# Optimization experiments

Measured on AMD Instinct MI355X. Metric: run time of the kernel, lower is better.

## Reference

```python
import jax, jax.numpy as jnp
import numpy as np

B, S, NUM_TYPES, NUM_NODES, FREQ = 8, 2048, 8, 32, 256
COMP_R, COMP_L, COMP_C = 0, 1, 2
LS = 0.1  # label smoothing
W_TYPE, W_NODE, W_VAL, W_IMP, W_D1, W_D2, W_SELF, W_DUP = 1.0, 1.0, 0.5, 1.0, 0.5, 0.3, 2.0, 1.0


def setup_inputs() -> dict:
    key = jax.random.key(0)
    ks = jax.random.split(key, 9)
    type_logits = jax.random.normal(ks[0], (B, S, NUM_TYPES), jnp.float32)
    node_a_logits = jax.random.normal(ks[1], (B, S, NUM_NODES), jnp.float32)
    node_b_logits = jax.random.normal(ks[2], (B, S, NUM_NODES), jnp.float32)
    values = jax.random.normal(ks[3], (B, S, 1), jnp.float32)
    t_type = jax.random.randint(ks[4], (B, S, 1), 0, NUM_TYPES)
    t_na = jax.random.randint(ks[5], (B, S, 1), 0, NUM_NODES)
    t_nb = jax.random.randint(ks[6], (B, S, 1), 0, NUM_NODES)
    t_val = jax.random.normal(ks[7], (B, S, 1), jnp.float32)
    target_seq = jnp.concatenate(
        [t_type.astype(jnp.float32), t_na.astype(jnp.float32), t_nb.astype(jnp.float32), t_val], axis=-1)
    ki = jax.random.split(ks[8], 2)
    pred_impedance = jax.random.normal(ki[0], (B, 2, FREQ), jnp.float32)
    target_impedance = jax.random.normal(ki[1], (B, 2, FREQ), jnp.float32)
    return {"type_logits": type_logits, "node_a_logits": node_a_logits,
            "node_b_logits": node_b_logits, "values": values, "target_seq": target_seq,
            "pred_impedance": pred_impedance, "target_impedance": target_impedance}


def _ce_smooth(logits, targets):
    # torch CrossEntropyLoss(label_smoothing=LS), mean reduction
    logp = jax.nn.log_softmax(logits, axis=-1)
    nll = -jnp.take_along_axis(logp, targets[..., None], axis=-1)[..., 0]
    smooth = -jnp.mean(logp, axis=-1)
    return jnp.mean((1.0 - LS) * nll + LS * smooth)


def _mse(a, b):
    return jnp.mean((a - b) ** 2)


def _losses(type_logits, node_a_logits, node_b_logits, values,
            pred_impedance, target_impedance, target_seq):
    target_types = target_seq[:, :, 0].astype(jnp.int32)
    target_na = target_seq[:, :, 1].astype(jnp.int32)
    target_nb = target_seq[:, :, 2].astype(jnp.int32)
    target_values = target_seq[:, :, 3:4]

    type_loss = _ce_smooth(type_logits, target_types)
    node_a_loss = _ce_smooth(node_a_logits, target_na)
    node_b_loss = _ce_smooth(node_b_logits, target_nb)
    value_loss = _mse(values, target_values)

    # validity penalties
    pa = jax.nn.softmax(node_a_logits, axis=-1)  # [B,S,N]
    pb = jax.nn.softmax(node_b_logits, axis=-1)
    pt = jax.nn.softmax(type_logits, axis=-1)
    comp_mask = pt[:, :, COMP_R] + pt[:, :, COMP_L] + pt[:, :, COMP_C]  # [B,S]

    selfloop_prob = jnp.sum(pa * pb, axis=-1)  # [B,S]
    selfloop_penalty = jnp.mean(selfloop_prob * comp_mask)

    # edge_probs[b,s] = outer(pa,pb) + outer(pa,pb).T, flattened to [B,S,N*N]
    outer = jnp.einsum('bsi,bsj->bsij', pa, pb)
    edge = (outer + jnp.swapaxes(outer, -1, -2)).reshape(B, S, NUM_NODES * NUM_NODES)
    em = edge * comp_mask[..., None]  # fold comp weight into edge vectors
    gram = jnp.einsum('bsk,btk->bst', em, em)  # [B,S,S]
    trace = jnp.einsum('bss->b', gram)
    pair_sum = 0.5 * (jnp.sum(gram) - jnp.sum(trace))
    duplicate_penalty = pair_sum / (B * S * (S - 1) / 2 + 1e-8)

    # impedance derivative losses
    pm, tm = pred_impedance[:, 0, :], target_impedance[:, 0, :]
    pp, tp = pred_impedance[:, 1, :], target_impedance[:, 1, :]
    mag_loss = _mse(pm, tm)
    pd1, td1 = pm[:, 1:] - pm[:, :-1], tm[:, 1:] - tm[:, :-1]
    d1_loss = _mse(pd1, td1)
    d2_loss = _mse(pd1[:, 1:] - pd1[:, :-1], td1[:, 1:] - td1[:, :-1])
    phase_loss = _mse(pp, tp)

    total = (W_TYPE * type_loss + W_NODE * (node_a_loss + node_b_loss)
             + W_VAL * value_loss + W_SELF * selfloop_penalty
             + W_DUP * duplicate_penalty + W_IMP * mag_loss
             + W_D1 * d1_loss + W_D2 * d2_loss + 0.1 * phase_loss)
    return (total, type_loss, node_a_loss, node_b_loss, value_loss,
            selfloop_penalty, duplicate_penalty, mag_loss, d1_loss, d2_loss, phase_loss)


def reference(type_logits, node_a_logits, node_b_logits, values, target_seq,
              pred_impedance, target_impedance):
    return _losses(type_logits, node_a_logits, node_b_logits, values,
                   pred_impedance, target_impedance, target_seq)
```

## Files before the change

kernel.cpp:

```cpp
#include <hip/hip_runtime.h>


#define BB 8
#define SS 2048
#define NT 8
#define NN 32
#define FQ 256
#define NPOS (BB*SS)
#define NBLK 256
#define WS_USLOT 0
#define WS_SSLOT (NBLK*1024)
#define WS_BATCH (WS_SSLOT + NBLK*8)

constexpr float LS_ = 0.1f;

__device__ __forceinline__ float softmax32(const float* __restrict__ src, int pos,
                                           int tgt, float* __restrict__ p) {
    const float4* q = reinterpret_cast<const float4*>(src) + pos * 8;
    #pragma unroll
    for (int i = 0; i < 8; i++) {
        float4 v = q[i];
        p[4*i] = v.x; p[4*i+1] = v.y; p[4*i+2] = v.z; p[4*i+3] = v.w;
    }
    float mx = p[0], sx = 0.f, pt = 0.f;
    #pragma unroll
    for (int i = 0; i < NN; i++) { mx = fmaxf(mx, p[i]); sx += p[i]; }
    #pragma unroll
    for (int i = 0; i < NN; i++) { pt = (i == tgt) ? p[i] : pt; }
    float es = 0.f;
    #pragma unroll
    for (int i = 0; i < NN; i++) { float e = expf(p[i] - mx); p[i] = e; es += e; }
    const float inv = 1.f / es;
    #pragma unroll
    for (int i = 0; i < NN; i++) p[i] *= inv;
    const float logZ = mx + logf(es);
    return (1.f - LS_) * (logZ - pt) + LS_ * (logZ - sx * (1.f / NN));
}

__global__ __launch_bounds__(64) void ck_main(
    const float* __restrict__ type_logits,
    const float* __restrict__ na_logits,
    const float* __restrict__ nb_logits,
    const float* __restrict__ values,
    const float* __restrict__ target_seq,
    float* __restrict__ ws)
{
    const int tid = threadIdx.x;
    const int bid = blockIdx.x;
    const int b   = bid >> 5;
    const int s   = ((bid & 31) << 6) + tid;
    const int pos = b * SS + s;

    const float4 tg = reinterpret_cast<const float4*>(target_seq)[pos];
    const int tt = (int)tg.x;
    const int ta = (int)tg.y;
    const int tb = (int)tg.z;
    const float tv = tg.w;

    float x[NT];
    {
        const float4* p = reinterpret_cast<const float4*>(type_logits) + pos * 2;
        float4 v0 = p[0], v1 = p[1];
        x[0]=v0.x; x[1]=v0.y; x[2]=v0.z; x[3]=v0.w;
        x[4]=v1.x; x[5]=v1.y; x[6]=v1.z; x[7]=v1.w;
    }
    float xmax = x[0], xs = 0.f, xt = 0.f;
    #pragma unroll
    for (int i = 0; i < NT; i++) { xmax = fmaxf(xmax, x[i]); xs += x[i]; }
    #pragma unroll
    for (int i = 0; i < NT; i++) { xt = (i == tt) ? x[i] : xt; }
    float es = 0.f, e012 = 0.f;
    #pragma unroll
    for (int i = 0; i < NT; i++) {
        float e = expf(x[i] - xmax);
        es += e;
        if (i < 3) e012 += e;
    }
    const float logZt = xmax + logf(es);
    const float lt = (1.f - LS_) * (logZt - xt) + LS_ * (logZt - xs * (1.f / NT));
    const float m = e012 / es;

    float pa[NN], pb[NN];
    const float la = softmax32(na_logits, pos, ta, pa);
    const float lb = softmax32(nb_logits, pos, tb, pb);

    float Sa = 0.f, Sb = 0.f, dot = 0.f;
    #pragma unroll
    for (int i = 0; i < NN; i++) {
        Sa = fmaf(pa[i], pa[i], Sa);
        Sb = fmaf(pb[i], pb[i], Sb);
        dot = fmaf(pa[i], pb[i], dot);
    }
    const float self = m * dot;
    const float tr   = 2.f * m * m * (Sa * Sb + dot * dot);
    const float dv   = values[pos] - tv;
    const float vsq  = dv * dv;

    float r0 = lt, r1 = la, r2 = lb, r3 = vsq, r4 = self, r5 = tr;
    #pragma unroll
    for (int o = 32; o > 0; o >>= 1) {
        r0 += __shfl_down(r0, o); r1 += __shfl_down(r1, o);
        r2 += __shfl_down(r2, o); r3 += __shfl_down(r3, o);
        r4 += __shfl_down(r4, o); r5 += __shfl_down(r5, o);
    }
    if (tid == 0) {
        float* sp = ws + WS_SSLOT + bid * 8;
        sp[0]=r0; sp[1]=r1; sp[2]=r2; sp[3]=r3; sp[4]=r4; sp[5]=r5;
    }

    __shared__ float4 lpa[64][9];
    __shared__ float4 lpb[64][9];
    #pragma unroll
    for (int q = 0; q < 8; q++) {
        lpa[tid][q] = make_float4(m*pa[4*q], m*pa[4*q+1], m*pa[4*q+2], m*pa[4*q+3]);
        lpb[tid][q] = make_float4(pb[4*q], pb[4*q+1], pb[4*q+2], pb[4*q+3]);
    }
    __syncthreads();

    const int i4 = tid >> 3;
    const int j4 = tid & 7;
    float acc[4][4];
    #pragma unroll
    for (int ii = 0; ii < 4; ii++)
        #pragma unroll
        for (int jj = 0; jj < 4; jj++) acc[ii][jj] = 0.f;
    for (int t = 0; t < 64; t++) {
        float4 av = lpa[t][i4];
        float4 bv = lpb[t][j4];
        const float aa[4] = {av.x, av.y, av.z, av.w};
        const float bbv[4] = {bv.x, bv.y, bv.z, bv.w};
        #pragma unroll
        for (int ii = 0; ii < 4; ii++)
            #pragma unroll
            for (int jj = 0; jj < 4; jj++)
                acc[ii][jj] = fmaf(aa[ii], bbv[jj], acc[ii][jj]);
    }
    float4* slot = reinterpret_cast<float4*>(ws + WS_USLOT + bid * 1024);
    #pragma unroll
    for (int ii = 0; ii < 4; ii++)
        slot[((i4*4+ii)*32 + j4*4) >> 2] =
            make_float4(acc[ii][0], acc[ii][1], acc[ii][2], acc[ii][3]);
}

__device__ __forceinline__ float blk_reduce256(float v, float* lds) {
    #pragma unroll
    for (int o = 32; o > 0; o >>= 1) v += __shfl_down(v, o);
    const int tid = threadIdx.x;
    __syncthreads();
    if ((tid & 63) == 0) lds[tid >> 6] = v;
    __syncthreads();
    return lds[0] + lds[1] + lds[2] + lds[3];
}

__global__ __launch_bounds__(256) void ck_batch(
    const float* __restrict__ pred_imp,
    const float* __restrict__ targ_imp,
    float* __restrict__ ws)
{
    const int tid = threadIdx.x;
    const int b   = blockIdx.x;
    __shared__ float Ub[1024];
    __shared__ float red[4];

    float ua = 0.f, ub = 0.f, uc = 0.f, ud = 0.f;
    const float* base = ws + WS_USLOT + (size_t)b * 32 * 1024;
    for (int sl = 0; sl < 32; sl++) {
        const float* p = base + sl * 1024;
        ua += p[tid];
        ub += p[tid + 256];
        uc += p[tid + 512];
        ud += p[tid + 768];
    }
    Ub[tid]       = ua;
    Ub[tid + 256] = ub;
    Ub[tid + 512] = uc;
    Ub[tid + 768] = ud;
    __syncthreads();

    float gr = 0.f;
    #pragma unroll
    for (int r = 0; r < 4; r++) {
        const int e = tid + r * 256;
        const int i = e >> 5, j = e & 31;
        const float u  = Ub[e];
        const float ut = Ub[(j << 5) | i];
        gr = fmaf(u, u, gr);
        gr = fmaf(u, ut, gr);
    }

    const float* pm = pred_imp + b * 2 * FQ;
    const float* tm = targ_imp + b * 2 * FQ;
    const int f = tid;
    const float p0 = pm[f], t0 = tm[f];
    const float dm = p0 - t0;
    const float dp = pm[FQ + f] - tm[FQ + f];
    float mag = dm * dm;
    float phs = dp * dp;
    float d1 = 0.f, d2 = 0.f;
    if (f < FQ - 1) {
        const float p1 = pm[f + 1], t1 = tm[f + 1];
        const float a = (p1 - p0) - (t1 - t0);
        d1 = a * a;
        if (f < FQ - 2) {
            const float p2 = pm[f + 2], t2 = tm[f + 2];
            const float c = (p2 - 2.f*p1 + p0) - (t2 - 2.f*t1 + t0);
            d2 = c * c;
        }
    }

    float s0=0.f, s1=0.f, s2=0.f, s3=0.f, s4=0.f, s5=0.f;
    if (tid < 32) {
        const float* sp = ws + WS_SSLOT + (b * 32 + tid) * 8;
        s0 = sp[0]; s1 = sp[1]; s2 = sp[2]; s3 = sp[3]; s4 = sp[4]; s5 = sp[5];
    }

    const float GR  = blk_reduce256(gr,  red);
    const float MAG = blk_reduce256(mag, red);
    const float PHS = blk_reduce256(phs, red);
    const float D1  = blk_reduce256(d1,  red);
    const float D2  = blk_reduce256(d2,  red);
    const float S0  = blk_reduce256(s0,  red);
    const float S1  = blk_reduce256(s1,  red);
    const float S2  = blk_reduce256(s2,  red);
    const float S3  = blk_reduce256(s3,  red);
    const float S4  = blk_reduce256(s4,  red);
    const float S5  = blk_reduce256(s5,  red);

    if (tid == 0) {
        float* o = ws + WS_BATCH + b * 16;
        o[0]=GR; o[1]=MAG; o[2]=PHS; o[3]=D1; o[4]=D2;
        o[5]=S0; o[6]=S1; o[7]=S2; o[8]=S3; o[9]=S4; o[10]=S5;
    }
}

__global__ __launch_bounds__(64) void ck_out(const float* __restrict__ ws,
                                             float* __restrict__ out)
{
    if (threadIdx.x != 0) return;
    float GR=0,MAG=0,PHS=0,D1=0,D2=0,S0=0,S1=0,S2=0,S3=0,S4=0,S5=0;
    #pragma unroll
    for (int b = 0; b < BB; b++) {
        const float* p = ws + WS_BATCH + b * 16;
        GR+=p[0]; MAG+=p[1]; PHS+=p[2]; D1+=p[3]; D2+=p[4];
        S0+=p[5]; S1+=p[6]; S2+=p[7]; S3+=p[8]; S4+=p[9]; S5+=p[10];
    }
    const float invN = 1.f / (float)NPOS;
    const float type_loss = S0 * invN;
    const float na_loss   = S1 * invN;
    const float nb_loss   = S2 * invN;
    const float val_loss  = S3 * invN;
    const float self_p    = S4 * invN;
    const float trace     = S5;
    const float sum_gram  = 2.f * GR;
    const float pair_sum  = 0.5f * (sum_gram - trace);
    const float dup   = pair_sum / ((float)BB * SS * (SS - 1) * 0.5f + 1e-8f);
    const float mag_l = MAG / (float)(BB * FQ);
    const float d1_l  = D1  / (float)(BB * (FQ - 1));
    const float d2_l  = D2  / (float)(BB * (FQ - 2));
    const float ph_l  = PHS / (float)(BB * FQ);
    const float total = 1.0f * type_loss + 1.0f * (na_loss + nb_loss)
                      + 0.5f * val_loss + 2.0f * self_p + 1.0f * dup
                      + 1.0f * mag_l + 0.5f * d1_l + 0.3f * d2_l + 0.1f * ph_l;
    out[0]=total; out[1]=type_loss; out[2]=na_loss; out[3]=nb_loss;
    out[4]=val_loss; out[5]=self_p; out[6]=dup; out[7]=mag_l;
    out[8]=d1_l; out[9]=d2_l; out[10]=ph_l;
}

extern "C" void kernel_launch(void* const* d_in, const int* in_sizes, int n_in,
                              void* d_out, int out_size, void* d_ws, size_t ws_size,
                              hipStream_t stream)
{
    const float* type_logits = (const float*)d_in[0];
    const float* na_logits   = (const float*)d_in[1];
    const float* nb_logits   = (const float*)d_in[2];
    const float* values      = (const float*)d_in[3];
    const float* target_seq  = (const float*)d_in[4];
    const float* pred_imp    = (const float*)d_in[5];
    const float* targ_imp    = (const float*)d_in[6];
    float* out = (float*)d_out;
    float* ws  = (float*)d_ws;

    ck_main<<<NBLK, 64, 0, stream>>>(type_logits, na_logits, nb_logits,
                                     values, target_seq, ws);
    ck_batch<<<BB, 256, 0, stream>>>(pred_imp, targ_imp, ws);
    ck_out<<<1, 64, 0, stream>>>(ws, out);
}
```

Measured before the change: 81.35 us.

## Fold final reduction into batch kernel via atomic ticket; pack two waves per block

Removes the third single-thread output kernel by having the last finishing batch block (detected with an atomic ticket counter plus thread fences) compute the final losses. ck_main now runs two independent wavefronts per 128-thread block, halving the block count while keeping per-wave slot layout. The intent is to cut one kernel launch and its inter-kernel gap. It adds a reset of the ticket inside ck_main and relies on correct fence ordering across blocks.

New measurement: 83.65 us. 1.03x slower.

```diff
diff --git a/kernel.cpp b/kernel.cpp
--- a/kernel.cpp
+++ b/kernel.cpp
@@ -7,10 +7,11 @@
 #define NN 32
 #define FQ 256
 #define NPOS (BB*SS)
-#define NBLK 256
+#define NSLOT 256
 #define WS_USLOT 0
-#define WS_SSLOT (NBLK*1024)
-#define WS_BATCH (WS_SSLOT + NBLK*8)
+#define WS_SSLOT (NSLOT*1024)
+#define WS_BATCH (WS_SSLOT + NSLOT*8)
+#define WS_TICKET (WS_BATCH + BB*16)
 
 constexpr float LS_ = 0.1f;
 
@@ -37,7 +38,7 @@
     return (1.f - LS_) * (logZ - pt) + LS_ * (logZ - sx * (1.f / NN));
 }
 
-__global__ __launch_bounds__(64) void ck_main(
+__global__ __launch_bounds__(128) void ck_main(
     const float* __restrict__ type_logits,
     const float* __restrict__ na_logits,
     const float* __restrict__ nb_logits,
@@ -45,11 +46,18 @@
     const float* __restrict__ target_seq,
     float* __restrict__ ws)
 {
-    const int tid = threadIdx.x;
-    const int bid = blockIdx.x;
-    const int b   = bid >> 5;
-    const int s   = ((bid & 31) << 6) + tid;
-    const int pos = b * SS + s;
+    const int tid  = threadIdx.x;
+    const int bid  = blockIdx.x;
+    const int w    = tid >> 6;
+    const int lane = tid & 63;
+    const int gw   = bid * 2 + w;
+    const int b    = gw >> 5;
+    const int s    = ((gw & 31) << 6) + lane;
+    const int pos  = b * SS + s;
+
+    if (tid == 0 && bid == 0) {
+        *reinterpret_cast<int*>(ws + WS_TICKET) = 0;
+    }
 
     const float4 tg = reinterpret_cast<const float4*>(target_seq)[pos];
     const int tt = (int)tg.x;
@@ -103,30 +111,30 @@
         r2 += __shfl_down(r2, o); r3 += __shfl_down(r3, o);
         r4 += __shfl_down(r4, o); r5 += __shfl_down(r5, o);
     }
-    if (tid == 0) {
-        float* sp = ws + WS_SSLOT + bid * 8;
+    if (lane == 0) {
+        float* sp = ws + WS_SSLOT + gw * 8;
         sp[0]=r0; sp[1]=r1; sp[2]=r2; sp[3]=r3; sp[4]=r4; sp[5]=r5;
     }
 
-    __shared__ float4 lpa[64][9];
-    __shared__ float4 lpb[64][9];
+    __shared__ float4 lpa[2][64][9];
+    __shared__ float4 lpb[2][64][9];
     #pragma unroll
     for (int q = 0; q < 8; q++) {
-        lpa[tid][q] = make_float4(m*pa[4*q], m*pa[4*q+1], m*pa[4*q+2], m*pa[4*q+3]);
-        lpb[tid][q] = make_float4(pb[4*q], pb[4*q+1], pb[4*q+2], pb[4*q+3]);
-    }
-    __syncthreads();
-
-    const int i4 = tid >> 3;
-    const int j4 = tid & 7;
+        lpa[w][lane][q] = make_float4(m*pa[4*q], m*pa[4*q+1], m*pa[4*q+2], m*pa[4*q+3]);
+        lpb[w][lane][q] = make_float4(pb[4*q], pb[4*q+1], pb[4*q+2], pb[4*q+3]);
+    }
+    __syncthreads();
+
+    const int i4 = lane >> 3;
+    const int j4 = lane & 7;
     float acc[4][4];
     #pragma unroll
     for (int ii = 0; ii < 4; ii++)
         #pragma unroll
         for (int jj = 0; jj < 4; jj++) acc[ii][jj] = 0.f;
     for (int t = 0; t < 64; t++) {
-        float4 av = lpa[t][i4];
-        float4 bv = lpb[t][j4];
+        float4 av = lpa[w][t][i4];
+        float4 bv = lpb[w][t][j4];
         const float aa[4] = {av.x, av.y, av.z, av.w};
         const float bbv[4] = {bv.x, bv.y, bv.z, bv.w};
         #pragma unroll
@@ -135,7 +143,7 @@
             for (int jj = 0; jj < 4; jj++)
                 acc[ii][jj] = fmaf(aa[ii], bbv[jj], acc[ii][jj]);
     }
-    float4* slot = reinterpret_cast<float4*>(ws + WS_USLOT + bid * 1024);
+    float4* slot = reinterpret_cast<float4*>(ws + WS_USLOT + gw * 1024);
     #pragma unroll
     for (int ii = 0; ii < 4; ii++)
         slot[((i4*4+ii)*32 + j4*4) >> 2] =
@@ -155,7 +163,8 @@
 __global__ __launch_bounds__(256) void ck_batch(
     const float* __restrict__ pred_imp,
     const float* __restrict__ targ_imp,
-    float* __restrict__ ws)
+    float* __restrict__ ws,
+    float* __restrict__ out)
 {
     const int tid = threadIdx.x;
     const int b   = blockIdx.x;
@@ -230,40 +239,41 @@
         float* o = ws + WS_BATCH + b * 16;
         o[0]=GR; o[1]=MAG; o[2]=PHS; o[3]=D1; o[4]=D2;
         o[5]=S0; o[6]=S1; o[7]=S2; o[8]=S3; o[9]=S4; o[10]=S5;
-    }
-}
-
-__global__ __launch_bounds__(64) void ck_out(const float* __restrict__ ws,
-                                             float* __restrict__ out)
-{
-    if (threadIdx.x != 0) return;
-    float GR=0,MAG=0,PHS=0,D1=0,D2=0,S0=0,S1=0,S2=0,S3=0,S4=0,S5=0;
-    #pragma unroll
-    for (int b = 0; b < BB; b++) {
-        const float* p = ws + WS_BATCH + b * 16;
-        GR+=p[0]; MAG+=p[1]; PHS+=p[2]; D1+=p[3]; D2+=p[4];
-        S0+=p[5]; S1+=p[6]; S2+=p[7]; S3+=p[8]; S4+=p[9]; S5+=p[10];
-    }
-    const float invN = 1.f / (float)NPOS;
-    const float type_loss = S0 * invN;
-    const float na_loss   = S1 * invN;
-    const float nb_loss   = S2 * invN;
-    const float val_loss  = S3 * invN;
-    const float self_p    = S4 * invN;
-    const float trace     = S5;
-    const float sum_gram  = 2.f * GR;
-    const float pair_sum  = 0.5f * (sum_gram - trace);
-    const float dup   = pair_sum / ((float)BB * SS * (SS - 1) * 0.5f + 1e-8f);
-    const float mag_l = MAG / (float)(BB * FQ);
-    const float d1_l  = D1  / (float)(BB * (FQ - 1));
-    const float d2_l  = D2  / (float)(BB * (FQ - 2));
-    const float ph_l  = PHS / (float)(BB * FQ);
-    const float total = 1.0f * type_loss + 1.0f * (na_loss + nb_loss)
-                      + 0.5f * val_loss + 2.0f * self_p + 1.0f * dup
-                      + 1.0f * mag_l + 0.5f * d1_l + 0.3f * d2_l + 0.1f * ph_l;
-    out[0]=total; out[1]=type_loss; out[2]=na_loss; out[3]=nb_loss;
-    out[4]=val_loss; out[5]=self_p; out[6]=dup; out[7]=mag_l;
-    out[8]=d1_l; out[9]=d2_l; out[10]=ph_l;
+
+        __threadfence();
+        int* ticket = reinterpret_cast<int*>(ws + WS_TICKET);
+        const int old = atomicAdd(ticket, 1);
+        if (old == BB - 1) {
+            __threadfence();
+            float GRt=0,MAGt=0,PHSt=0,D1t=0,D2t=0,T0=0,T1=0,T2=0,T3=0,T4=0,T5=0;
+            #pragma unroll
+            for (int k = 0; k < BB; k++) {
+                const float* p = ws + WS_BATCH + k * 16;
+                GRt+=p[0]; MAGt+=p[1]; PHSt+=p[2]; D1t+=p[3]; D2t+=p[4];
+                T0+=p[5]; T1+=p[6]; T2+=p[7]; T3+=p[8]; T4+=p[9]; T5+=p[10];
+            }
+            const float invN = 1.f / (float)NPOS;
+            const float type_loss = T0 * invN;
+            const float na_loss   = T1 * invN;
+            const float nb_loss   = T2 * invN;
+            const float val_loss  = T3 * invN;
+            const float self_p    = T4 * invN;
+            const float trace     = T5;
+            const float sum_gram  = 2.f * GRt;
+            const float pair_sum  = 0.5f * (sum_gram - trace);
+            const float dup   = pair_sum / ((float)BB * SS * (SS - 1) * 0.5f + 1e-8f);
+            const float mag_l = MAGt / (float)(BB * FQ);
+            const float d1_l  = D1t  / (float)(BB * (FQ - 1));
+            const float d2_l  = D2t  / (float)(BB * (FQ - 2));
+            const float ph_l  = PHSt / (float)(BB * FQ);
+            const float total = 1.0f * type_loss + 1.0f * (na_loss + nb_loss)
+                              + 0.5f * val_loss + 2.0f * self_p + 1.0f * dup
+                              + 1.0f * mag_l + 0.5f * d1_l + 0.3f * d2_l + 0.1f * ph_l;
+            out[0]=total; out[1]=type_loss; out[2]=na_loss; out[3]=nb_loss;
+            out[4]=val_loss; out[5]=self_p; out[6]=dup; out[7]=mag_l;
+            out[8]=d1_l; out[9]=d2_l; out[10]=ph_l;
+        }
+    }
 }
 
 extern "C" void kernel_launch(void* const* d_in, const int* in_sizes, int n_in,
@@ -280,8 +290,7 @@
     float* out = (float*)d_out;
     float* ws  = (float*)d_ws;
 
-    ck_main<<<NBLK, 64, 0, stream>>>(type_logits, na_logits, nb_logits,
+    ck_main<<<128, 128, 0, stream>>>(type_logits, na_logits, nb_logits,
                                      values, target_seq, ws);
-    ck_batch<<<BB, 256, 0, stream>>>(pred_imp, targ_imp, ws);
-    ck_out<<<1, 64, 0, stream>>>(ws, out);
-}
+    ck_batch<<<BB, 256, 0, stream>>>(pred_imp, targ_imp, ws, out);
+}
```
